# Performance work log

Measured on AMD Instinct MI355X. Metric: run time of the kernel, lower is better.

## Reference

```python
import jax, jax.numpy as jnp
import numpy as np

N = 100000
E = 1600000
K = 3
DIMS = [64, 64, 64, 32, 16]


def setup_inputs() -> dict:
    key = jax.random.key(0)
    ks = jax.random.split(key, 12)
    inp = {
        "x": jax.random.normal(ks[0], (N, DIMS[0]), jnp.float32),
        "edge_index": jax.random.randint(ks[1], (2, E), 0, N, dtype=jnp.int64),
        "edge_weight": jax.random.uniform(ks[2], (E,), jnp.float32),
    }
    for i in range(4):
        scale = 1.0 / np.sqrt(DIMS[i] * K).astype(np.float32)
        inp[f"W{i+1}"] = jax.random.normal(ks[3 + 2 * i], (K, DIMS[i], DIMS[i + 1]), jnp.float32) * scale
        inp[f"b{i+1}"] = jnp.zeros((DIMS[i + 1],), jnp.float32)
    return inp


def _cheb_norm(edge_index, edge_weight, n):
    # PyG ChebConv norm with normalization='sym', lambda_max=2:
    # L = I - D^{-1/2} A D^{-1/2}; L_hat = 2L/lambda_max - I = -D^{-1/2} A D^{-1/2} (zero diag)
    row, col = edge_index[0], edge_index[1]
    w = jnp.where(row == col, 0.0, edge_weight)  # remove self loops
    deg = jax.ops.segment_sum(w, row, num_segments=n)
    dinv = jnp.where(deg > 0, jax.lax.rsqrt(deg), 0.0)  # inf -> 0 masking
    return -dinv[row] * w * dinv[col]


def _cheb_conv(x, edge_index, norm, W, b):
    row, col = edge_index[0], edge_index[1]
    n = x.shape[0]

    def prop(t):  # sparse L_hat @ t via gather + segment scatter-add
        return jax.ops.segment_sum(norm[:, None] * t[row], col, num_segments=n)

    Tx0 = x
    out = Tx0 @ W[0]
    Tx1 = prop(Tx0)
    out = out + Tx1 @ W[1]
    for k in range(2, W.shape[0]):
        Tx2 = 2.0 * prop(Tx1) - Tx0  # Chebyshev recurrence
        out = out + Tx2 @ W[k]
        Tx0, Tx1 = Tx1, Tx2
    return out + b


def reference(x, edge_index, edge_weight, W1, b1, W2, b2, W3, b3, W4, b4):
    norm = _cheb_norm(edge_index, edge_weight, x.shape[0])
    h = x
    for W, b in ((W1, b1), (W2, b2), (W3, b3), (W4, b4)):
        h = jax.nn.sigmoid(_cheb_conv(h, edge_index, norm, W, b))
    return h
```

## Files before the change

### kernel.cpp

```cpp
#include <hip/hip_runtime.h>
#include <math.h>


typedef __attribute__((ext_vector_type(8))) short short8_t;
typedef __attribute__((ext_vector_type(4))) short short4_t;
typedef __attribute__((ext_vector_type(4))) float f32x4;

#define NPP 256
#define CHUNK 2048

__device__ __forceinline__ float bf2f(short s) {
    return __int_as_float(((int)(unsigned short)s) << 16);
}
__device__ __forceinline__ short f2bf(float f) {
    unsigned u = __float_as_uint(f);
    return (short)((u + 0x7FFFu + ((u >> 16) & 1u)) >> 16);
}


__global__ __launch_bounds__(256) void f2b_kernel(
        const float* __restrict__ in, short* __restrict__ out, long m) {
    long i = ((long)blockIdx.x * 256 + threadIdx.x) * 4;
    if (i >= m) return;
    float4 v = *reinterpret_cast<const float4*>(in + i);
    short4_t s;
    s[0] = f2bf(v.x); s[1] = f2bf(v.y); s[2] = f2bf(v.z); s[3] = f2bf(v.w);
    *reinterpret_cast<short4_t*>(out + i) = s;
}


__global__ __launch_bounds__(256) void prep_kernel(
        const float* __restrict__ W1, const float* __restrict__ W2,
        const float* __restrict__ W3, const float* __restrict__ W4,
        short8_t* __restrict__ wpk1, short8_t* __restrict__ wpk2,
        short8_t* __restrict__ wpkm, short8_t* __restrict__ wpk4) {
    int idx = blockIdx.x * 256 + threadIdx.x;
    if (idx >= 4032) return;
    short8_t out;
    if (idx < 3072) {
        const float* W = (idx < 1536) ? W1 : W2;
        int f = (idx < 1536) ? idx : idx - 1536;
        int lane = f & 63, ct = (f >> 6) & 3, s = f >> 8;
        int li = lane & 15, lg = lane >> 4;
        int p = s >> 1;
        int col = ct * 16 + li;
#pragma unroll
        for (int e = 0; e < 8; ++e) {
            int k = (s & 1) * 32 + lg * 8 + e;
            int base = k * 64 + col;
            float v = (p == 0) ? W[base] - W[8192 + base]
                    : (p == 1) ? W[4096 + base]
                               : 2.0f * W[8192 + base];
            out[e] = f2bf(v);
        }
        ((idx < 1536) ? wpk1 : wpk2)[f] = out;
    } else if (idx < 3840) {
        int f = idx - 3072;
        int lane = f & 63, q = f >> 6;
        int s = q / 6, ct = q % 6;
        int li = lane & 15, lg = lane >> 4;
        int g = ct >> 1;
        int cl = (ct & 1) * 16 + li;
#pragma unroll
        for (int e = 0; e < 8; ++e) {
            int k = s * 32 + lg * 8 + e;
            int base = k * 32 + cl;
            float v = (g == 0) ? W3[base] - W3[4096 + base]
                    : (g == 1) ? W3[2048 + base]
                               : W3[4096 + base];
            out[e] = f2bf(v);
        }
        wpkm[f] = out;
    } else {
        int f = idx - 3840;
        int lane = f & 63, s = f >> 6;
        int li = lane & 15, lg = lane >> 4;
#pragma unroll
        for (int e = 0; e < 8; ++e) {
            int k = lg * 8 + e;
            int base = k * 16 + li;
            float v = (s == 0) ? W4[base] - W4[1024 + base]
                    : (s == 1) ? W4[512 + base]
                               : 2.0f * W4[1024 + base];
            out[e] = f2bf(v);
        }
        wpk4[f] = out;
    }
}


__global__ __launch_bounds__(256) void count_kernel(
        const int* __restrict__ row, const int* __restrict__ col,
        int* __restrict__ cntC, int* __restrict__ cntR, int P, int E) {
    __shared__ int hc[2][512], hr[2][512];
    for (int i = threadIdx.x; i < P; i += 256) {
        hc[0][i] = 0; hc[1][i] = 0; hr[0][i] = 0; hr[1][i] = 0;
    }
    __syncthreads();
    int cp = threadIdx.x & 1;
    int base = blockIdx.x * CHUNK;
    int lim = min(E, base + CHUNK);
    for (int e = base + threadIdx.x; e < lim; e += 256) {
        atomicAdd(&hc[cp][col[e] >> 8], 1);
        atomicAdd(&hr[cp][row[e] >> 8], 1);
    }
    __syncthreads();
    long o = (long)blockIdx.x * P;
    for (int i = threadIdx.x; i < P; i += 256) {
        cntC[o + i] = hc[0][i] + hc[1][i];
        cntR[o + i] = hr[0][i] + hr[1][i];
    }
}

__global__ __launch_bounds__(256) void colscan_kernel(
        int* __restrict__ cntC, int* __restrict__ cntR,
        int* __restrict__ ptotC, int* __restrict__ ptotR, int P, int B) {
    int bid = blockIdx.x;
    int* m; int* ptot; int p;
    if (bid < P) { m = cntC; ptot = ptotC; p = bid; }
    else         { m = cntR; ptot = ptotR; p = bid - P; }
    __shared__ int sh[256];
    int run = 0;
    for (int b0 = 0; b0 < B; b0 += 256) {
        int b = b0 + threadIdx.x;
        int v = (b < B) ? m[(long)b * P + p] : 0;
        sh[threadIdx.x] = v;
        __syncthreads();
        for (int o = 1; o < 256; o <<= 1) {
            int t = (threadIdx.x >= o) ? sh[threadIdx.x - o] : 0;
            __syncthreads();
            sh[threadIdx.x] += t;
            __syncthreads();
        }
        if (b < B) m[(long)b * P + p] = run + sh[threadIdx.x] - v;
        run += sh[255];
        __syncthreads();
    }
    if (threadIdx.x == 0) ptot[p] = run;
}

__global__ __launch_bounds__(512) void pscan_kernel(
        const int* __restrict__ ptotC, const int* __restrict__ ptotR,
        int* __restrict__ pofsC, int* __restrict__ pofsR,
        int* __restrict__ ofs, int P, int n, int E) {
    __shared__ int sh[512];
    int tid = threadIdx.x;
    int v = (tid < P) ? ptotC[tid] : 0;
    sh[tid] = v;
    __syncthreads();
    for (int o = 1; o < 512; o <<= 1) {
        int t = (tid >= o) ? sh[tid - o] : 0;
        __syncthreads();
        sh[tid] += t;
        __syncthreads();
    }
    if (tid < P) pofsC[tid] = sh[tid] - v;
    if (tid == 0) pofsC[P] = E;
    __syncthreads();
    v = (tid < P) ? ptotR[tid] : 0;
    sh[tid] = v;
    __syncthreads();
    for (int o = 1; o < 512; o <<= 1) {
        int t = (tid >= o) ? sh[tid - o] : 0;
        __syncthreads();
        sh[tid] += t;
        __syncthreads();
    }
    if (tid < P) pofsR[tid] = sh[tid] - v;
    if (tid == 0) { pofsR[P] = E; ofs[n] = E; }
}

__global__ __launch_bounds__(256) void scatter_kernel(
        const int* __restrict__ row, const int* __restrict__ col,
        const float* __restrict__ ew,
        const int* __restrict__ cntC, const int* __restrict__ cntR,
        const int* __restrict__ pofsC, const int* __restrict__ pofsR,
        int2* __restrict__ bufC, unsigned* __restrict__ bufR, int P, int E) {
    __shared__ int hc[512], hr[512];
    long o = (long)blockIdx.x * P;
    for (int i = threadIdx.x; i < P; i += 256) {
        hc[i] = pofsC[i] + cntC[o + i];
        hr[i] = pofsR[i] + cntR[o + i];
    }
    __syncthreads();
    int base = blockIdx.x * CHUNK;
    int lim = min(E, base + CHUNK);
    for (int e = base + threadIdx.x; e < lim; e += 256) {
        int r = row[e], c = col[e];
        float w = (r == c) ? 0.0f : ew[e];
        unsigned wb = __float_as_uint(w);
        int pc = atomicAdd(&hc[c >> 8], 1);
        bufC[pc] = make_int2((int)(((unsigned)(c & 255) << 24) | (unsigned)r), (int)wb);
        int pr = atomicAdd(&hr[r >> 8], 1);
        bufR[pr] = ((unsigned)(r & 255) << 24) | (wb >> 8);
    }
}

__global__ __launch_bounds__(256) void dinv_kernel(
        const unsigned* __restrict__ bufR, const int* __restrict__ rofs,
        float* __restrict__ dinv, int n) {
    int p = blockIdx.x;
    __shared__ float s[NPP];
    s[threadIdx.x] = 0.0f;
    __syncthreads();
    int beg = rofs[p], end = rofs[p + 1];
    for (int k = beg + threadIdx.x; k < end; k += 256) {
        unsigned u = bufR[k];
        atomicAdd(&s[u >> 24], __uint_as_float((u & 0xFFFFFFu) << 8));
    }
    __syncthreads();
    int node = (p << 8) + threadIdx.x;
    if (node < n) {
        float d = s[threadIdx.x];
        dinv[node] = d > 0.0f ? rsqrtf(d) : 0.0f;
    }
}

__global__ __launch_bounds__(256) void fine_csr_kernel(
        const int2* __restrict__ bufC, const int* __restrict__ pofs,
        const float* __restrict__ dinv, int* __restrict__ ofs,
        int2* __restrict__ epk, int n) {
    int p = blockIdx.x;
    int tid = threadIdx.x;
    __shared__ int hist[NPP];
    __shared__ int sc[NPP];
    __shared__ float dc[NPP];
    hist[tid] = 0;
    int node = (p << 8) + tid;
    dc[tid] = (node < n) ? dinv[node] : 0.0f;
    __syncthreads();
    int beg = pofs[p], end = pofs[p + 1];
    for (int k = beg + tid; k < end; k += 256)
        atomicAdd(&hist[((unsigned)bufC[k].x) >> 24], 1);
    __syncthreads();
    int v = hist[tid];
    sc[tid] = v;
    __syncthreads();
    for (int o = 1; o < 256; o <<= 1) {
        int t = (tid >= o) ? sc[tid - o] : 0;
        __syncthreads();
        sc[tid] += t;
        __syncthreads();
    }
    int mybase = beg + sc[tid] - v;
    if (node < n) ofs[node] = mybase;
    hist[tid] = mybase;
    __syncthreads();
    for (int k = beg + tid; k < end; k += 256) {
        int2 ed = bufC[k];
        unsigned key = (unsigned)ed.x;
        int fc = key >> 24;
        int r = (int)(key & 0xFFFFFFu);
        float w = __int_as_float(ed.y);
        float nrm = -dinv[r] * w * dc[fc];
        int pos = atomicAdd(&hist[fc], 1);
        epk[pos] = make_int2(r, __float_as_int(nrm));
    }
}


template <int D>
__global__ __launch_bounds__(256) void agg_kernel(
        const int* __restrict__ ofs, const int2* __restrict__ epk,
        const short* __restrict__ tb, short* __restrict__ outb, int n) {
    constexpr int LPN = D / 8;
    int idx = blockIdx.x * 256 + threadIdx.x;
    int node = idx / LPN;
    int l = idx % LPN;
    if (node >= n) return;
    int beg = ofs[node], end = ofs[node + 1];
    float a[8] = {0.f, 0.f, 0.f, 0.f, 0.f, 0.f, 0.f, 0.f};
    const short* tc = tb + l * 8;
    int k = beg;
    for (; k + 4 <= end; k += 4) {
        int2 ev[4];
        short8_t xv[4];
#pragma unroll
        for (int u = 0; u < 4; ++u) ev[u] = epk[k + u];
#pragma unroll
        for (int u = 0; u < 4; ++u)
            xv[u] = *reinterpret_cast<const short8_t*>(tc + (long)ev[u].x * D);
#pragma unroll
        for (int u = 0; u < 4; ++u) {
            float v = __int_as_float(ev[u].y);
#pragma unroll
            for (int j = 0; j < 8; ++j) a[j] = fmaf(v, bf2f(xv[u][j]), a[j]);
        }
    }
    for (; k < end; ++k) {
        int2 e0 = epk[k];
        short8_t x0 = *reinterpret_cast<const short8_t*>(tc + (long)e0.x * D);
        float v = __int_as_float(e0.y);
#pragma unroll
        for (int j = 0; j < 8; ++j) a[j] = fmaf(v, bf2f(x0[j]), a[j]);
    }
    short8_t s;
#pragma unroll
    for (int j = 0; j < 8; ++j) s[j] = f2bf(a[j]);
    *reinterpret_cast<short8_t*>(outb + (long)node * D + l * 8) = s;
}


__global__ __launch_bounds__(256) void agg_dual_kernel(
        const int* __restrict__ ofs, const int2* __restrict__ epk,
        const short* __restrict__ tb, short* __restrict__ Q1b,
        short* __restrict__ Q2b, int n) {
    int idx = blockIdx.x * 256 + threadIdx.x;
    int node = idx >> 3;
    int l = idx & 7;
    if (node >= n) return;
    int beg = ofs[node], end = ofs[node + 1];
    float a[8] = {0.f, 0.f, 0.f, 0.f, 0.f, 0.f, 0.f, 0.f};
    const short* tc = tb + l * 8;
    int k = beg;
    for (; k + 4 <= end; k += 4) {
        int2 ev[4];
        short8_t xv[4];
#pragma unroll
        for (int u = 0; u < 4; ++u) ev[u] = epk[k + u];
#pragma unroll
        for (int u = 0; u < 4; ++u)
            xv[u] = *reinterpret_cast<const short8_t*>(tc + (long)ev[u].x * 64);
#pragma unroll
        for (int u = 0; u < 4; ++u) {
            float v = __int_as_float(ev[u].y);
#pragma unroll
            for (int j = 0; j < 8; ++j) a[j] = fmaf(v, bf2f(xv[u][j]), a[j]);
        }
    }
    for (; k < end; ++k) {
        int2 e0 = epk[k];
        short8_t x0 = *reinterpret_cast<const short8_t*>(tc + (long)e0.x * 64);
        float v = __int_as_float(e0.y);
#pragma unroll
        for (int j = 0; j < 8; ++j) a[j] = fmaf(v, bf2f(x0[j]), a[j]);
    }
    short* ob = (l < 4) ? Q1b : Q2b;
    long o = (long)node * 32 + (l & 3) * 8;
    short8_t s;
#pragma unroll
    for (int j = 0; j < 8; ++j) s[j] = f2bf(a[j]);
    *reinterpret_cast<short8_t*>(ob + o) = s;
}


__global__ __launch_bounds__(256) void agg_fin_kernel(
        const int* __restrict__ ofs, const int2* __restrict__ epk,
        const short* __restrict__ Q2b, const float* __restrict__ S,
        const short* __restrict__ Q1b, short* __restrict__ outb, int n) {
    int idx = blockIdx.x * 256 + threadIdx.x;
    int node = idx >> 2;
    int l = idx & 3;
    if (node >= n) return;
    int beg = ofs[node], end = ofs[node + 1];
    float a[8] = {0.f, 0.f, 0.f, 0.f, 0.f, 0.f, 0.f, 0.f};
    const short* tc = Q2b + l * 8;
    int k = beg;
    for (; k + 4 <= end; k += 4) {
        int2 ev[4];
        short8_t xv[4];
#pragma unroll
        for (int u = 0; u < 4; ++u) ev[u] = epk[k + u];
#pragma unroll
        for (int u = 0; u < 4; ++u)
            xv[u] = *reinterpret_cast<const short8_t*>(tc + (long)ev[u].x * 32);
#pragma unroll
        for (int u = 0; u < 4; ++u) {
            float v = __int_as_float(ev[u].y);
#pragma unroll
            for (int j = 0; j < 8; ++j) a[j] = fmaf(v, bf2f(xv[u][j]), a[j]);
        }
    }
    for (; k < end; ++k) {
        int2 e0 = epk[k];
        short8_t x0 = *reinterpret_cast<const short8_t*>(tc + (long)e0.x * 32);
        float v = __int_as_float(e0.y);
#pragma unroll
        for (int j = 0; j < 8; ++j) a[j] = fmaf(v, bf2f(x0[j]), a[j]);
    }
    long o = (long)node * 32 + l * 8;
    float4 s0 = *reinterpret_cast<const float4*>(S + o);
    float4 s1 = *reinterpret_cast<const float4*>(S + o + 4);
    short8_t q1 = *reinterpret_cast<const short8_t*>(Q1b + o);
    float sv[8] = {s0.x, s0.y, s0.z, s0.w, s1.x, s1.y, s1.z, s1.w};
    short8_t r;
#pragma unroll
    for (int j = 0; j < 8; ++j) {
        float z = sv[j] + bf2f(q1[j]) + 2.0f * a[j];
        r[j] = f2bf(1.0f / (1.0f + expf(-z)));
    }
    *reinterpret_cast<short8_t*>(outb + o) = r;
}


__global__ __launch_bounds__(256) void gemm3_mfma(
        const short* __restrict__ t0b, const short* __restrict__ t1b,
        const short* __restrict__ t2b, const short8_t* __restrict__ wpk,
        const float* __restrict__ b, short* __restrict__ outb, int n) {
    const int tid = threadIdx.x;
    const int wave = tid >> 6;
    const int lane = tid & 63;
    const int li = lane & 15;
    const int lg = lane >> 4;

    short8_t bfr[6][4];
#pragma unroll
    for (int s = 0; s < 6; ++s)
#pragma unroll
        for (int ct = 0; ct < 4; ++ct)
            bfr[s][ct] = wpk[(s * 4 + ct) * 64 + lane];

    float bias_v[4];
#pragma unroll
    for (int ct = 0; ct < 4; ++ct) bias_v[ct] = b[ct * 16 + li];

#pragma unroll
    for (int t = 0; t < 2; ++t) {
        int r0 = blockIdx.x * 128 + wave * 32 + t * 16;
        if (r0 >= n) continue;
        int rA = r0 + li;
        if (rA >= n) rA = n - 1;
        f32x4 acc[4] = {{0.f, 0.f, 0.f, 0.f}, {0.f, 0.f, 0.f, 0.f},
                        {0.f, 0.f, 0.f, 0.f}, {0.f, 0.f, 0.f, 0.f}};
#pragma unroll
        for (int s = 0; s < 6; ++s) {
            const short* src = (s < 2) ? t0b : (s < 4) ? t1b : t2b;
            int k = (s & 1) * 32 + lg * 8;
            short8_t a = *reinterpret_cast<const short8_t*>(src + (long)rA * 64 + k);
#pragma unroll
            for (int ct = 0; ct < 4; ++ct)
                acc[ct] = __builtin_amdgcn_mfma_f32_16x16x32_bf16(a, bfr[s][ct], acc[ct], 0, 0, 0);
        }
#pragma unroll
        for (int ct = 0; ct < 4; ++ct) {
#pragma unroll
            for (int reg = 0; reg < 4; ++reg) {
                int row = r0 + lg * 4 + reg;
                if (row < n) {
                    float z = acc[ct][reg] + bias_v[ct];
                    float res = 1.0f / (1.0f + expf(-z));
                    outb[(long)row * 64 + ct * 16 + li] = f2bf(res);
                }
            }
        }
    }
}


__global__ __launch_bounds__(256) void gemm_multi_mfma(
        const short* __restrict__ hb, const short8_t* __restrict__ wpk,
        const float* __restrict__ b, short* __restrict__ P12b,
        float* __restrict__ S, int n) {
    const int tid = threadIdx.x;
    const int wave = tid >> 6;
    const int lane = tid & 63;
    const int li = lane & 15;
    const int lg = lane >> 4;

    short8_t bfr[2][6];
#pragma unroll
    for (int s = 0; s < 2; ++s)
#pragma unroll
        for (int ct = 0; ct < 6; ++ct)
            bfr[s][ct] = wpk[(s * 6 + ct) * 64 + lane];

    float bS0 = b[li], bS1 = b[16 + li];

#pragma unroll
    for (int t = 0; t < 2; ++t) {
        int r0 = blockIdx.x * 128 + wave * 32 + t * 16;
        if (r0 >= n) continue;
        int rA = r0 + li;
        if (rA >= n) rA = n - 1;
        f32x4 acc[6] = {{0.f, 0.f, 0.f, 0.f}, {0.f, 0.f, 0.f, 0.f},
                        {0.f, 0.f, 0.f, 0.f}, {0.f, 0.f, 0.f, 0.f},
                        {0.f, 0.f, 0.f, 0.f}, {0.f, 0.f, 0.f, 0.f}};
#pragma unroll
        for (int s = 0; s < 2; ++s) {
            int k = s * 32 + lg * 8;
            short8_t a = *reinterpret_cast<const short8_t*>(hb + (long)rA * 64 + k);
#pragma unroll
            for (int ct = 0; ct < 6; ++ct)
                acc[ct] = __builtin_amdgcn_mfma_f32_16x16x32_bf16(a, bfr[s][ct], acc[ct], 0, 0, 0);
        }
#pragma unroll
        for (int ct = 0; ct < 6; ++ct) {
            int g = ct >> 1;
            int cl = (ct & 1) * 16 + li;
#pragma unroll
            for (int reg = 0; reg < 4; ++reg) {
                int row = r0 + lg * 4 + reg;
                if (row >= n) continue;
                float v = acc[ct][reg];
                if (g == 0) {
                    S[(long)row * 32 + cl] = v + ((ct & 1) ? bS1 : bS0);
                } else if (g == 1) {
                    P12b[(long)row * 64 + cl] = f2bf(v);
                } else {
                    P12b[(long)row * 64 + 32 + cl] = f2bf(v);
                }
            }
        }
    }
}


__global__ __launch_bounds__(256) void gemm4_mfma(
        const short* __restrict__ t0b, const short* __restrict__ t1b,
        const short* __restrict__ t2b, const short8_t* __restrict__ wpk,
        const float* __restrict__ b, float* __restrict__ out, int n) {
    const int tid = threadIdx.x;
    const int wave = tid >> 6;
    const int lane = tid & 63;
    const int li = lane & 15;
    const int lg = lane >> 4;

    short8_t bfr[3];
#pragma unroll
    for (int s = 0; s < 3; ++s) bfr[s] = wpk[s * 64 + lane];

    float bias_v = b[li];

#pragma unroll
    for (int t = 0; t < 2; ++t) {
        int r0 = blockIdx.x * 128 + wave * 32 + t * 16;
        if (r0 >= n) continue;
        int rA = r0 + li;
        if (rA >= n) rA = n - 1;
        f32x4 acc = {0.f, 0.f, 0.f, 0.f};
        int k = lg * 8;
        short8_t a0 = *reinterpret_cast<const short8_t*>(t0b + (long)rA * 32 + k);
        acc = __builtin_amdgcn_mfma_f32_16x16x32_bf16(a0, bfr[0], acc, 0, 0, 0);
        short8_t a1 = *reinterpret_cast<const short8_t*>(t1b + (long)rA * 32 + k);
        acc = __builtin_amdgcn_mfma_f32_16x16x32_bf16(a1, bfr[1], acc, 0, 0, 0);
        short8_t a2 = *reinterpret_cast<const short8_t*>(t2b + (long)rA * 32 + k);
        acc = __builtin_amdgcn_mfma_f32_16x16x32_bf16(a2, bfr[2], acc, 0, 0, 0);
#pragma unroll
        for (int reg = 0; reg < 4; ++reg) {
            int row = r0 + lg * 4 + reg;
            if (row < n) {
                float z = acc[reg] + bias_v;
                out[(long)row * 16 + li] = 1.0f / (1.0f + expf(-z));
            }
        }
    }
}


static inline int ceil_div_l(long a, long b) { return (int)((a + b - 1) / b); }

extern "C" void kernel_launch(void* const* d_in, const int* in_sizes, int n_in,
                              void* d_out, int out_size, void* d_ws, size_t ws_size,
                              hipStream_t stream) {
    const float* x  = (const float*)d_in[0];
    const int*   ei = (const int*)d_in[1];
    const float* ew = (const float*)d_in[2];
    const float* W1 = (const float*)d_in[3];  const float* b1 = (const float*)d_in[4];
    const float* W2 = (const float*)d_in[5];  const float* b2 = (const float*)d_in[6];
    const float* W3 = (const float*)d_in[7];  const float* b3 = (const float*)d_in[8];
    const float* W4 = (const float*)d_in[9];  const float* b4 = (const float*)d_in[10];

    const int E = in_sizes[2];
    const int n = in_sizes[0] / 64;
    const int* row = ei;
    const int* col = ei + E;
    const int P = (n + NPP - 1) / NPP;
    const int B = (E + CHUNK - 1) / CHUNK;

    char* ws = (char*)d_ws;
    size_t off = 0;
    auto alloc = [&](size_t bytes) -> void* {
        void* p = ws + off;
        off += (bytes + 255) & ~(size_t)255;
        return p;
    };
    int*      cntC = (int*)alloc((size_t)B * P * sizeof(int));
    int*      cntR = (int*)alloc((size_t)B * P * sizeof(int));
    int*      ptotC = (int*)alloc(512 * sizeof(int));
    int*      ptotR = (int*)alloc(512 * sizeof(int));
    int*      pofsC = (int*)alloc((512 + 1) * sizeof(int));
    int*      pofsR = (int*)alloc((512 + 1) * sizeof(int));
    float*    dinv = (float*)alloc((size_t)n * sizeof(float));
    int*      ofs  = (int*)alloc((size_t)(n + 1) * sizeof(int));
    int2*     bufC = (int2*)alloc((size_t)E * sizeof(int2));
    unsigned* bufR = (unsigned*)alloc((size_t)E * sizeof(unsigned));
    int2*     epk  = (int2*)alloc((size_t)E * sizeof(int2));
    short*    hbA  = (short*)alloc((size_t)n * 64 * sizeof(short));
    short*    hbB  = (short*)alloc((size_t)n * 64 * sizeof(short));
    short*    t1b  = (short*)alloc((size_t)n * 64 * sizeof(short));
    short*    Ub   = (short*)alloc((size_t)n * 64 * sizeof(short));
    float*    S    = (float*)alloc((size_t)n * 32 * sizeof(float));
    short8_t* wpk1 = (short8_t*)alloc(1536 * sizeof(short8_t));
    short8_t* wpk2 = (short8_t*)alloc(1536 * sizeof(short8_t));
    short8_t* wpkm = (short8_t*)alloc(768 * sizeof(short8_t));
    short8_t* wpk4 = (short8_t*)alloc(192 * sizeof(short8_t));
    if (off > ws_size) return;

    f2b_kernel<<<ceil_div_l((long)n * 16, 256), 256, 0, stream>>>(x, hbA, (long)n * 64);
    prep_kernel<<<16, 256, 0, stream>>>(W1, W2, W3, W4, wpk1, wpk2, wpkm, wpk4);

    count_kernel<<<B, 256, 0, stream>>>(row, col, cntC, cntR, P, E);
    colscan_kernel<<<2 * P, 256, 0, stream>>>(cntC, cntR, ptotC, ptotR, P, B);
    pscan_kernel<<<1, 512, 0, stream>>>(ptotC, ptotR, pofsC, pofsR, ofs, P, n, E);
    scatter_kernel<<<B, 256, 0, stream>>>(row, col, ew, cntC, cntR, pofsC, pofsR,
                                          bufC, bufR, P, E);
    dinv_kernel<<<P, 256, 0, stream>>>(bufR, pofsR, dinv, n);
    fine_csr_kernel<<<P, 256, 0, stream>>>(bufC, pofsC, dinv, ofs, epk, n);

    const int ab64 = ceil_div_l((long)n * 8, 256);
    const int ab32 = ceil_div_l((long)n * 4, 256);
    const int gb = ceil_div_l(n, 128);

    agg_kernel<64><<<ab64, 256, 0, stream>>>(ofs, epk, hbA, t1b, n);
    agg_kernel<64><<<ab64, 256, 0, stream>>>(ofs, epk, t1b, Ub, n);
    gemm3_mfma<<<gb, 256, 0, stream>>>(hbA, t1b, Ub, wpk1, b1, hbB, n);

    agg_kernel<64><<<ab64, 256, 0, stream>>>(ofs, epk, hbB, t1b, n);
    agg_kernel<64><<<ab64, 256, 0, stream>>>(ofs, epk, t1b, Ub, n);
    gemm3_mfma<<<gb, 256, 0, stream>>>(hbB, t1b, Ub, wpk2, b2, hbA, n);

    {
        short* P12b = t1b;
        short* Q1b  = Ub;
        short* Q2b  = Ub + (size_t)n * 32;
        short* hb3  = hbB;
        gemm_multi_mfma<<<gb, 256, 0, stream>>>(hbA, wpkm, b3, P12b, S, n);
        agg_dual_kernel<<<ab64, 256, 0, stream>>>(ofs, epk, P12b, Q1b, Q2b, n);
        agg_fin_kernel<<<ab32, 256, 0, stream>>>(ofs, epk, Q2b, S, Q1b, hb3, n);
    }

    agg_kernel<32><<<ab32, 256, 0, stream>>>(ofs, epk, hbB, t1b, n);
    agg_kernel<32><<<ab32, 256, 0, stream>>>(ofs, epk, t1b, Ub, n);
    gemm4_mfma<<<gb, 256, 0, stream>>>(hbB, t1b, Ub, wpk4, b4, (float*)d_out, n);
}
```

Measured before the change: 396.9 us.

## Enlarge scatter chunk, use nontemporal bucket stores, unroll aggregation gathers by eight

The edge-bucketing kernel now handles larger chunks per block (CHUNK 8192 instead of 2048) and writes its bucket entries with nontemporal stores, aiming to cut per-block histogram overhead and keep these streaming writes out of cache. Both aggregation kernels gain an 8-way unrolled gather loop ahead of the existing 4-way one, putting more independent row loads in flight per lane. The costs are fewer blocks for the bucketing pass, since each block now covers four times the edges, and more registers in the aggregation kernels, which may lower occupancy.

```diff
diff --git a/kernel.cpp b/kernel.cpp
--- a/kernel.cpp
+++ b/kernel.cpp
@@ -7,7 +7,7 @@
 typedef __attribute__((ext_vector_type(4))) float f32x4;
 
 #define NPP 256
-#define CHUNK 2048
+#define CHUNK 8192
 
 __device__ __forceinline__ float bf2f(short s) {
     return __int_as_float(((int)(unsigned short)s) << 16);
@@ -190,9 +190,11 @@
         float w = (r == c) ? 0.0f : ew[e];
         unsigned wb = __float_as_uint(w);
         int pc = atomicAdd(&hc[c >> 8], 1);
-        bufC[pc] = make_int2((int)(((unsigned)(c & 255) << 24) | (unsigned)r), (int)wb);
+        union { int2 i2; long long ll; } u;
+        u.i2 = make_int2((int)(((unsigned)(c & 255) << 24) | (unsigned)r), (int)wb);
+        __builtin_nontemporal_store(u.ll, reinterpret_cast<long long*>(&bufC[pc]));
         int pr = atomicAdd(&hr[r >> 8], 1);
-        bufR[pr] = ((unsigned)(r & 255) << 24) | (wb >> 8);
+        __builtin_nontemporal_store(((unsigned)(r & 255) << 24) | (wb >> 8), &bufR[pr]);
     }
 }
 
@@ -272,6 +274,21 @@
     float a[8] = {0.f, 0.f, 0.f, 0.f, 0.f, 0.f, 0.f, 0.f};
     const short* tc = tb + l * 8;
     int k = beg;
+    for (; k + 8 <= end; k += 8) {
+        int2 ev[8];
+        short8_t xv[8];
+#pragma unroll
+        for (int u = 0; u < 8; ++u) ev[u] = epk[k + u];
+#pragma unroll
+        for (int u = 0; u < 8; ++u)
+            xv[u] = *reinterpret_cast<const short8_t*>(tc + (long)ev[u].x * D);
+#pragma unroll
+        for (int u = 0; u < 8; ++u) {
+            float v = __int_as_float(ev[u].y);
+#pragma unroll
+            for (int j = 0; j < 8; ++j) a[j] = fmaf(v, bf2f(xv[u][j]), a[j]);
+        }
+    }
     for (; k + 4 <= end; k += 4) {
         int2 ev[4];
         short8_t xv[4];
@@ -313,6 +330,21 @@
     float a[8] = {0.f, 0.f, 0.f, 0.f, 0.f, 0.f, 0.f, 0.f};
     const short* tc = tb + l * 8;
     int k = beg;
+    for (; k + 8 <= end; k += 8) {
+        int2 ev[8];
+        short8_t xv[8];
+#pragma unroll
+        for (int u = 0; u < 8; ++u) ev[u] = epk[k + u];
+#pragma unroll
+        for (int u = 0; u < 8; ++u)
+            xv[u] = *reinterpret_cast<const short8_t*>(tc + (long)ev[u].x * 64);
+#pragma unroll
+        for (int u = 0; u < 8; ++u) {
+            float v = __int_as_float(ev[u].y);
+#pragma unroll
+            for (int j = 0; j < 8; ++j) a[j] = fmaf(v, bf2f(xv[u][j]), a[j]);
+        }
+    }
     for (; k + 4 <= end; k += 4) {
         int2 ev[4];
         short8_t xv[4];
@@ -446,7 +478,6 @@
     }
 }
 
-
 __global__ __launch_bounds__(256) void gemm_multi_mfma(
         const short* __restrict__ hb, const short8_t* __restrict__ wpk,
         const float* __restrict__ b, short* __restrict__ P12b,
@@ -503,7 +534,6 @@
         }
     }
 }
-
 
 __global__ __launch_bounds__(256) void gemm4_mfma(
         const short* __restrict__ t0b, const short* __restrict__ t1b,
```

New measurement: 456.5 us. +15.0%, slower.
